# Optimization experiments

Measured on AMD Instinct MI355X. Metric: run time of the kernel, lower is better.

The kernel has to match this reference:

```python
import jax, jax.numpy as jnp
import numpy as np

B, IMG, P, D, H, HD, DEPTH, MLPD = 32, 224, 16, 768, 12, 64, 12, 3072
N = (IMG // P) ** 2 + 1  # 197 tokens incl. cls
TASKS, PL, NPL = 10, 5, 5
SCALE = HD ** -0.5


def _ln(x, w, b, eps=1e-6):
    m = jnp.mean(x, -1, keepdims=True)
    v = jnp.var(x, -1, keepdims=True)
    return (x - m) * jax.lax.rsqrt(v + eps) * w + b


def setup_inputs():
    key = jax.random.key(0)
    ks = jax.random.split(key, 16)
    g = lambda k, shape: (jax.random.normal(k, shape) * 0.02).astype(jnp.float32)
    return dict(
        x=jax.random.normal(ks[0], (B, 3, IMG, IMG), jnp.float32),
        task_id=jax.random.randint(ks[1], (B,), 0, TASKS),
        patch_w=g(ks[2], (D, 3, P, P)), patch_b=jnp.zeros((D,), jnp.float32),
        cls_token=g(ks[3], (1, 1, D)), pos_embed=g(ks[4], (1, N, D)),
        ln1_w=jnp.ones((DEPTH, D)), ln1_b=jnp.zeros((DEPTH, D)),
        qkv_w=g(ks[5], (DEPTH, 3 * D, D)), qkv_b=jnp.zeros((DEPTH, 3 * D)),
        proj_w=g(ks[6], (DEPTH, D, D)), proj_b=jnp.zeros((DEPTH, D)),
        ln2_w=jnp.ones((DEPTH, D)), ln2_b=jnp.zeros((DEPTH, D)),
        fc1_w=g(ks[7], (DEPTH, MLPD, D)), fc1_b=jnp.zeros((DEPTH, MLPD)),
        fc2_w=g(ks[8], (DEPTH, D, MLPD)), fc2_b=jnp.zeros((DEPTH, D)),
        norm_w=jnp.ones((D,)), norm_b=jnp.zeros((D,)),
        prefix_k=g(ks[9], (NPL, TASKS, PL, H, HD)),
        prefix_v=g(ks[10], (NPL, TASKS, PL, H, HD)),
        act_scale=jnp.ones((NPL, 2, 1, 1), jnp.float32),
    )


def reference(x, task_id, patch_w, patch_b, cls_token, pos_embed, ln1_w, ln1_b,
              qkv_w, qkv_b, proj_w, proj_b, ln2_w, ln2_b, fc1_w, fc1_b,
              fc2_w, fc2_b, norm_w, norm_b, prefix_k, prefix_v, act_scale):
    tid = jnp.clip(task_id, 0, TASKS - 1)
    Bx = x.shape[0]
    # patch embed: conv stride P -> [B, D, 14, 14] -> [B, 196, D]
    h = jax.lax.conv_general_dilated(x, patch_w, (P, P), 'VALID',
                                     dimension_numbers=('NCHW', 'OIHW', 'NCHW'))
    h = h.reshape(Bx, D, -1).transpose(0, 2, 1) + patch_b
    h = jnp.concatenate([jnp.broadcast_to(cls_token, (Bx, 1, D)), h], axis=1)
    h = h + pos_embed
    for i in range(DEPTH):
        xn = _ln(h, ln1_w[i], ln1_b[i])
        qkv = (xn @ qkv_w[i].T + qkv_b[i]).reshape(Bx, N, 3, H, HD)
        q, k, v = [jnp.transpose(qkv[:, :, j], (0, 2, 1, 3)) for j in range(3)]  # [B,H,N,HD]
        if i < NPL:
            kp = jnp.transpose(prefix_k[i][tid], (0, 2, 1, 3))  # [B,H,PL,HD]
            vp = jnp.transpose(prefix_v[i][tid], (0, 2, 1, 3))
            k = jnp.concatenate([kp, k], axis=2)
            v = jnp.concatenate([vp, v], axis=2)
        logits = jnp.einsum('bhqd,bhkd->bhqk', q, k) * SCALE
        if i < NPL:
            s = act_scale[i]  # [2,1,1]
            pp = logits[..., :PL]
            pp = pp + jax.nn.sigmoid(pp * s[0]) * s[1]  # norga gating on prefix logits
            logits = jnp.concatenate([pp, logits[..., PL:]], axis=-1)
        probs = jax.nn.softmax(logits, axis=-1)
        attn = jnp.einsum('bhqk,bhkd->bhqd', probs, v)
        attn = attn.transpose(0, 2, 1, 3).reshape(Bx, N, D)
        h = h + attn @ proj_w[i].T + proj_b[i]
        yn = _ln(h, ln2_w[i], ln2_b[i])
        y = jax.nn.gelu(yn @ fc1_w[i].T + fc1_b[i], approximate=False)
        h = h + y @ fc2_w[i].T + fc2_b[i]
    h = _ln(h, norm_w, norm_b)
    return h[:, 0]
```

## Files before the change

kernel.cpp:

```cpp
#include <hip/hip_runtime.h>
#include <hip/hip_bf16.h>

#define B_     32
#define NTOK   197
#define NPATCH 196
#define D_     768
#define H_     12
#define HD_    64
#define DEPTH_ 12
#define MLPD_  3072
#define TASKS_ 10
#define PL_    5
#define NPL_   5
#define SCALE_ 0.125f
#define ROWS   (B_*NTOK)
#define PSZ    (ROWS*D_)

typedef unsigned short ushortT;
typedef __bf16 bf16x8 __attribute__((ext_vector_type(8)));
typedef float  f32x4  __attribute__((ext_vector_type(4)));
typedef unsigned int u32x4 __attribute__((ext_vector_type(4)));

union FragU { u32x4 u; bf16x8 b; };

__device__ inline unsigned int f2bf(float f){
  unsigned int u = __float_as_uint(f);
  return (u + 0x7fffu + ((u >> 16) & 1u)) >> 16;
}
__device__ inline float bf2f(ushortT u){ return __uint_as_float(((unsigned)u) << 16); }
__device__ inline float gelu_f(float x){ return 0.5f * x * (1.f + erff(x * 0.70710678118f)); }

__device__ inline void gload16(const void* g, void* l){
  __builtin_amdgcn_global_load_lds(
      (const __attribute__((address_space(1))) void*)(uintptr_t)g,
      (__attribute__((address_space(3))) void*)(uintptr_t)l,
      16, 0, 0);
}

#define DSREAD(dst, addr, OFFS) \
  asm volatile("ds_read_b128 %0, %1 offset:" OFFS : "=v"(dst) : "v"(addr))

__global__ __launch_bounds__(256) void convw4_kernel(const float* __restrict__ s0,
    const float* __restrict__ s1, const float* __restrict__ s2, const float* __restrict__ s3,
    ushortT* __restrict__ dst)
{
  int idx = blockIdx.x * 256 + threadIdx.x;
  int e = idx * 8;
  if (e >= 7077888) return;
  const float* s; int loc;
  if (e < 1769472)      { s = s0; loc = e; }
  else if (e < 2359296) { s = s1; loc = e - 1769472; }
  else if (e < 4718592) { s = s2; loc = e - 2359296; }
  else                  { s = s3; loc = e - 4718592; }
  float4 a = *(const float4*)(s + loc);
  float4 c = *(const float4*)(s + loc + 4);
  uint4 o;
  o.x = f2bf(a.x) | (f2bf(a.y) << 16);
  o.y = f2bf(a.z) | (f2bf(a.w) << 16);
  o.z = f2bf(c.x) | (f2bf(c.y) << 16);
  o.w = f2bf(c.z) | (f2bf(c.w) << 16);
  *(uint4*)(dst + e) = o;
}

__global__ __launch_bounds__(256) void convw1_kernel(const float* __restrict__ s,
    ushortT* __restrict__ dst, int n8)
{
  int idx = blockIdx.x * 256 + threadIdx.x;
  if (idx >= n8) return;
  int e = idx * 8;
  float4 a = *(const float4*)(s + e);
  float4 c = *(const float4*)(s + e + 4);
  uint4 o;
  o.x = f2bf(a.x) | (f2bf(a.y) << 16);
  o.y = f2bf(a.z) | (f2bf(a.w) << 16);
  o.z = f2bf(c.x) | (f2bf(c.y) << 16);
  o.w = f2bf(c.z) | (f2bf(c.w) << 16);
  *(uint4*)(dst + e) = o;
}

__global__ __launch_bounds__(256) void im2col_kernel(const float* __restrict__ x,
                                                     ushortT* __restrict__ out)
{
  int idx = blockIdx.x * 256 + threadIdx.x;
  const int tot = B_ * NPATCH * D_;
  if (idx >= tot) return;
  int m = idx / D_, k = idx - m * D_;
  int b = m / NPATCH, p = m - b * NPATCH;
  int pr = p / 14, pc = p - pr * 14;
  int c = k >> 8, r = k & 255;
  int py = r >> 4, px = r & 15;
  float v = x[(((size_t)(b * 3 + c) * 224) + pr * 16 + py) * 224 + pc * 16 + px];
  out[idx] = (ushortT)f2bf(v);
}

__global__ __launch_bounds__(256) void assemble_ln_kernel(const float* __restrict__ pe,
    const float* __restrict__ patch_b, const float* __restrict__ cls,
    const float* __restrict__ pos, float* __restrict__ h,
    const float* __restrict__ lw, const float* __restrict__ lb,
    ushortT* __restrict__ y)
{
  const int row = blockIdx.x;
  const int b = row / NTOK, n = row - b * NTOK;
  const size_t base = (size_t)row * D_;
  const int t = threadIdx.x;
  float vals[3];
  float s = 0.f, ss = 0.f;
  #pragma unroll
  for (int e = 0; e < 3; e++) {
    int d = t + e * 256;
    float v;
    if (n == 0) v = cls[d];
    else        v = pe[((size_t)b * NPATCH + (n - 1)) * D_ + d] + patch_b[d];
    v += pos[(size_t)n * D_ + d];
    h[base + d] = v;
    vals[e] = v; s += v; ss += v * v;
  }
  #pragma unroll
  for (int off = 32; off >= 1; off >>= 1) {
    s  += __shfl_down(s, off);
    ss += __shfl_down(ss, off);
  }
  __shared__ float sm[4], ssm[4];
  int wid = t >> 6, lane = t & 63;
  if (lane == 0) { sm[wid] = s; ssm[wid] = ss; }
  __syncthreads();
  s  = sm[0] + sm[1] + sm[2] + sm[3];
  ss = ssm[0] + ssm[1] + ssm[2] + ssm[3];
  float mean = s * (1.f / D_);
  float var  = ss * (1.f / D_) - mean * mean;
  float inv  = rsqrtf(var + 1e-6f);
  #pragma unroll
  for (int e = 0; e < 3; e++) {
    int d = t + e * 256;
    y[base + d] = (ushortT)f2bf((vals[e] - mean) * inv * lw[d] + lb[d]);
  }
}

template<int NP, int DOLN>
__global__ __launch_bounds__(256) void reduce_ln_kernel(
    const ushortT* __restrict__ p, const float* __restrict__ bias,
    float* __restrict__ h, const float* __restrict__ lw,
    const float* __restrict__ lb, ushortT* __restrict__ y)
{
  const size_t base = (size_t)blockIdx.x * D_;
  const int t = threadIdx.x;
  float vals[3];
  float s = 0.f, ss = 0.f;
  #pragma unroll
  for (int e = 0; e < 3; e++) {
    int d = t + e * 256;
    size_t idx = base + d;
    float acc = h[idx] + bias[d];
    #pragma unroll
    for (int q = 0; q < NP; q++) acc += bf2f(p[(size_t)q * PSZ + idx]);
    h[idx] = acc;
    vals[e] = acc; s += acc; ss += acc * acc;
  }
  if (DOLN) {
    #pragma unroll
    for (int off = 32; off >= 1; off >>= 1) {
      s  += __shfl_down(s, off);
      ss += __shfl_down(ss, off);
    }
    __shared__ float sm[4], ssm[4];
    int wid = t >> 6, lane = t & 63;
    if (lane == 0) { sm[wid] = s; ssm[wid] = ss; }
    __syncthreads();
    s  = sm[0] + sm[1] + sm[2] + sm[3];
    ss = ssm[0] + ssm[1] + ssm[2] + ssm[3];
    float mean = s * (1.f / D_);
    float var  = ss * (1.f / D_) - mean * mean;
    float inv  = rsqrtf(var + 1e-6f);
    #pragma unroll
    for (int e = 0; e < 3; e++) {
      int d = t + e * 256;
      y[base + d] = (ushortT)f2bf((vals[e] - mean) * inv * lw[d] + lb[d]);
    }
  }
}

template<int OUTBF>
__global__ __launch_bounds__(256) void ln_kernel(const float* __restrict__ x, size_t xstride,
    const float* __restrict__ w, const float* __restrict__ b,
    void* __restrict__ y, size_t ystride)
{
  const float* xr = x + (size_t)blockIdx.x * xstride;
  float vals[3];
  float s = 0.f, ss = 0.f;
  #pragma unroll
  for (int t = 0; t < 3; t++) {
    float v = xr[threadIdx.x + t * 256];
    vals[t] = v; s += v; ss += v * v;
  }
  #pragma unroll
  for (int off = 32; off >= 1; off >>= 1) {
    s  += __shfl_down(s, off);
    ss += __shfl_down(ss, off);
  }
  __shared__ float sm[4], ssm[4];
  int wid = threadIdx.x >> 6, lane = threadIdx.x & 63;
  if (lane == 0) { sm[wid] = s; ssm[wid] = ss; }
  __syncthreads();
  s  = sm[0] + sm[1] + sm[2] + sm[3];
  ss = ssm[0] + ssm[1] + ssm[2] + ssm[3];
  float mean = s * (1.f / D_);
  float var  = ss * (1.f / D_) - mean * mean;
  float inv  = rsqrtf(var + 1e-6f);
  #pragma unroll
  for (int t = 0; t < 3; t++) {
    int d = threadIdx.x + t * 256;
    float v = (vals[t] - mean) * inv * w[d] + b[d];
    if (OUTBF) ((ushortT*)y)[(size_t)blockIdx.x * ystride + d] = (ushortT)f2bf(v);
    else       ((float*)y)  [(size_t)blockIdx.x * ystride + d] = v;
  }
}

template<int OUTBF, int ACT, int HASRES>
__global__ __launch_bounds__(256, 6) void gemm_mfma(
    const ushortT* __restrict__ A, const ushortT* __restrict__ W,
    const float* __restrict__ bias, const float* __restrict__ resid,
    void* __restrict__ Cout, int M, int N, int K, int LDA, int LDW)
{
  __shared__ ushortT lds[12288];
  const int tid = threadIdx.x, lane = tid & 63, wid = tid >> 6;
  const int bm = blockIdx.y * 128, bn = blockIdx.x * 64;
  const int wm = (wid >> 1) * 64, wn = (wid & 1) * 32;
  const int kz = blockIdx.z;
  A += (size_t)kz * K; W += (size_t)kz * K;
  char* Cb = (char*)Cout + (size_t)kz * M * N * (OUTBF ? 2 : 4);

  const int srow = lane >> 2;
  const int scol = ((lane & 3) ^ ((lane >> 3) & 3)) * 8;
  int arow0 = bm + (2 * wid) * 16 + srow;     if (arow0 > M - 1) arow0 = M - 1;
  int arow1 = bm + (2 * wid + 1) * 16 + srow; if (arow1 > M - 1) arow1 = M - 1;
  const int wrow = bn + wid * 16 + srow;
  const ushortT* aP0 = A + (size_t)arow0 * LDA + scol;
  const ushortT* aP1 = A + (size_t)arow1 * LDA + scol;
  const ushortT* wP0 = W + (size_t)wrow * LDW + scol;
  ushortT* sA = lds + 2 * wid * 512;
  ushortT* sW = lds + 8192 + wid * 512;

  f32x4 acc[4][2];
  #pragma unroll
  for (int i = 0; i < 4; i++)
    #pragma unroll
    for (int j = 0; j < 2; j++)
      acc[i][j] = (f32x4){0.f, 0.f, 0.f, 0.f};

  const int rsel = lane & 15, kc = lane >> 4;
  const unsigned ldsbase = (unsigned)(size_t)&lds[0];
  const unsigned rowoff = (unsigned)(rsel * 64 + ((kc ^ ((rsel >> 1) & 3)) << 4));
  const unsigned aBase = ldsbase + (unsigned)(wm * 64) + rowoff;
  const unsigned bBase = ldsbase + 16384u + (unsigned)(wn * 64) + rowoff;

  const int nk = K >> 5;

  #pragma unroll
  for (int p = 0; p < 2; ++p) {
    const int off = p * 32;
    gload16(aP0 + off, sA + p * 4096); gload16(aP1 + off, sA + p * 4096 + 512);
    gload16(wP0 + off, sW + p * 2048);
  }

  for (int kt = 0; kt < nk; ++kt) {
    const int cb = kt & 1;
    asm volatile("s_waitcnt vmcnt(3)" ::: "memory");
    __builtin_amdgcn_sched_barrier(0);
    __builtin_amdgcn_s_barrier();

    const unsigned aAddr = aBase + (unsigned)cb * 8192u;
    const unsigned bAddr = bBase + (unsigned)cb * 4096u;
    FragU fa0, fa1, fa2, fa3, fb0, fb1;
    DSREAD(fa0.u, aAddr, "0");
    DSREAD(fa1.u, aAddr, "1024");
    DSREAD(fa2.u, aAddr, "2048");
    DSREAD(fa3.u, aAddr, "3072");
    DSREAD(fb0.u, bAddr, "0");
    DSREAD(fb1.u, bAddr, "1024");
    asm volatile("s_waitcnt lgkmcnt(0)" ::: "memory");
    __builtin_amdgcn_sched_barrier(0);
    __builtin_amdgcn_s_barrier();

    const int nt = kt + 2;
    const int off = (nt < nk) ? nt * 32 : 0;
    gload16(aP0 + off, sA + cb * 4096); gload16(aP1 + off, sA + cb * 4096 + 512);
    gload16(wP0 + off, sW + cb * 2048);

    acc[0][0] = __builtin_amdgcn_mfma_f32_16x16x32_bf16(fa0.b, fb0.b, acc[0][0], 0, 0, 0);
    acc[0][1] = __builtin_amdgcn_mfma_f32_16x16x32_bf16(fa0.b, fb1.b, acc[0][1], 0, 0, 0);
    acc[1][0] = __builtin_amdgcn_mfma_f32_16x16x32_bf16(fa1.b, fb0.b, acc[1][0], 0, 0, 0);
    acc[1][1] = __builtin_amdgcn_mfma_f32_16x16x32_bf16(fa1.b, fb1.b, acc[1][1], 0, 0, 0);
    acc[2][0] = __builtin_amdgcn_mfma_f32_16x16x32_bf16(fa2.b, fb0.b, acc[2][0], 0, 0, 0);
    acc[2][1] = __builtin_amdgcn_mfma_f32_16x16x32_bf16(fa2.b, fb1.b, acc[2][1], 0, 0, 0);
    acc[3][0] = __builtin_amdgcn_mfma_f32_16x16x32_bf16(fa3.b, fb0.b, acc[3][0], 0, 0, 0);
    acc[3][1] = __builtin_amdgcn_mfma_f32_16x16x32_bf16(fa3.b, fb1.b, acc[3][1], 0, 0, 0);
  }

  const int crow = (lane >> 4) * 4, ccol = lane & 15;
  #pragma unroll
  for (int i = 0; i < 4; i++) {
    #pragma unroll
    for (int r = 0; r < 4; r++) {
      int m = bm + wm + i * 16 + crow + r;
      if (m < M) {
        #pragma unroll
        for (int j = 0; j < 2; j++) {
          int n = bn + wn + j * 16 + ccol;
          float v = acc[i][j][r];
          if (bias) v += bias[n];
          if (ACT) v = gelu_f(v);
          if (HASRES) v += resid[(size_t)m * N + n];
          if (OUTBF) ((ushortT*)Cb)[(size_t)m * N + n] = (ushortT)f2bf(v);
          else       ((float*)Cb)  [(size_t)m * N + n] = v;
        }
      }
    }
  }
  asm volatile("s_waitcnt vmcnt(0)" ::: "memory");
}

#define KROWS 208
#define VSTR  232
__global__ __launch_bounds__(256) void attn_mfma(
    const ushortT* __restrict__ qkv, const float* __restrict__ prefix_k,
    const float* __restrict__ prefix_v, const float* __restrict__ act_scale,
    const int* __restrict__ task_id, ushortT* __restrict__ out,
    int layer, int koff)
{
  __shared__ ushortT smem[13312 + 14848 + 4096];
  ushortT* Kl = smem;
  ushortT* Vt = smem + 13312;
  ushortT* Ps = smem + 13312 + 14848;

  const int tid = threadIdx.x, lane = tid & 63, wid = tid >> 6;
  const int g = lane >> 4, qc = lane & 15;
  const int qh = blockIdx.x, h = blockIdx.y, b = blockIdx.z;
  const int KtA = NTOK + koff;

  int tsk = 0;
  float s0 = 1.f, s1 = 1.f;
  if (koff) {
    tsk = task_id[b]; tsk = tsk < 0 ? 0 : (tsk > TASKS_ - 1 ? TASKS_ - 1 : tsk);
    s0 = act_scale[layer * 2]; s1 = act_scale[layer * 2 + 1];
  }

  {
    uint4* vz = (uint4*)Vt;
    for (int i = tid; i < 14848 / 8; i += 256) vz[i] = (uint4){0, 0, 0, 0};
    uint4* kz = (uint4*)(Kl + 202 * 64);
    if (tid < 48) kz[tid] = (uint4){0, 0, 0, 0};
  }
  __syncthreads();

  for (int u = tid; u < KtA * 8; u += 256) {
    int row = u >> 3, cg = u & 7;
    uint4 val;
    if (row < koff) {
      size_t off = ((((size_t)layer * TASKS_ + tsk) * PL_ + row) * H_ + h) * HD_ + cg * 8;
      float4 f0 = *(const float4*)(prefix_k + off);
      float4 f1 = *(const float4*)(prefix_k + off + 4);
      val.x = f2bf(f0.x) | (f2bf(f0.y) << 16); val.y = f2bf(f0.z) | (f2bf(f0.w) << 16);
      val.z = f2bf(f1.x) | (f2bf(f1.y) << 16); val.w = f2bf(f1.z) | (f2bf(f1.w) << 16);
    } else {
      int n = row - koff;
      val = *(const uint4*)(qkv + ((size_t)b * NTOK + n) * 2304 + D_ + h * HD_ + cg * 8);
    }
    *(uint4*)(Kl + row * 64 + ((cg * 8) ^ ((row & 7) << 3))) = val;
  }
  for (int u = tid; u < KtA * 8; u += 256) {
    int row = u >> 3, dg = u & 7;
    ushortT e[8];
    if (row < koff) {
      size_t off = ((((size_t)layer * TASKS_ + tsk) * PL_ + row) * H_ + h) * HD_ + dg * 8;
      #pragma unroll
      for (int t = 0; t < 8; t++) e[t] = (ushortT)f2bf(prefix_v[off + t]);
    } else {
      int n = row - koff;
      uint4 v = *(const uint4*)(qkv + ((size_t)b * NTOK + n) * 2304 + 2 * D_ + h * HD_ + dg * 8);
      *(uint4*)e = v;
    }
    #pragma unroll
    for (int t = 0; t < 8; t++) Vt[(dg * 8 + t) * VSTR + row] = e[t];
  }
  __syncthreads();

  const int tend = qh ? 13 : 7;
  for (int t = qh * 7 + wid; t < tend; t += 4) {
    const int q0 = t * 16;
    int qr = q0 + qc; if (qr > NTOK - 1) qr = NTOK - 1;
    const ushortT* qp = qkv + ((size_t)b * NTOK + qr) * 2304 + h * HD_ + g * 8;
    bf16x8 qf0 = *(const bf16x8*)qp;
    bf16x8 qf1 = *(const bf16x8*)(qp + 32);

    f32x4 sacc[13];
    #pragma unroll
    for (int kt = 0; kt < 13; kt++) sacc[kt] = (f32x4){0.f, 0.f, 0.f, 0.f};
    #pragma unroll
    for (int kt = 0; kt < 13; kt++) {
      int row = kt * 16 + qc;
      int sw = (row & 7) << 3;
      bf16x8 ka0 = *(const bf16x8*)(Kl + row * 64 + ((g * 8) ^ sw));
      bf16x8 ka1 = *(const bf16x8*)(Kl + row * 64 + ((32 + g * 8) ^ sw));
      sacc[kt] = __builtin_amdgcn_mfma_f32_16x16x32_bf16(ka0, qf0, sacc[kt], 0, 0, 0);
      sacc[kt] = __builtin_amdgcn_mfma_f32_16x16x32_bf16(ka1, qf1, sacc[kt], 0, 0, 0);
    }

    float* sp = (float*)sacc;
    float mx = -1e30f;
    #pragma unroll
    for (int kt = 0; kt < 13; kt++)
      #pragma unroll
      for (int r = 0; r < 4; r++) {
        int k = kt * 16 + g * 4 + r;
        float s = sp[kt * 4 + r] * SCALE_;
        if (koff && k < PL_) s += s1 / (1.f + __expf(-s * s0));
        if (k >= KtA) s = -1e30f;
        sp[kt * 4 + r] = s;
        mx = fmaxf(mx, s);
      }
    mx = fmaxf(mx, __shfl_xor(mx, 16));
    mx = fmaxf(mx, __shfl_xor(mx, 32));
    float sum = 0.f;
    #pragma unroll
    for (int i = 0; i < 52; i++) { float p = __expf(sp[i] - mx); sp[i] = p; sum += p; }
    sum += __shfl_xor(sum, 16);
    sum += __shfl_xor(sum, 32);
    const float inv = 1.f / sum;

    f32x4 oacc[4];
    #pragma unroll
    for (int d = 0; d < 4; d++) oacc[d] = (f32x4){0.f, 0.f, 0.f, 0.f};
    #pragma unroll
    for (int c = 0; c < 7; c++) {
      ushortT* slab = Ps + wid * 1024 + (c & 1) * 512;
      uint2 w0, w1;
      {
        float p0 = sp[8 * c + 0] * inv, p1 = sp[8 * c + 1] * inv;
        float p2 = sp[8 * c + 2] * inv, p3 = sp[8 * c + 3] * inv;
        w0.x = f2bf(p0) | (f2bf(p1) << 16); w0.y = f2bf(p2) | (f2bf(p3) << 16);
      }
      if (c < 6) {
        float p0 = sp[8 * c + 4] * inv, p1 = sp[8 * c + 5] * inv;
        float p2 = sp[8 * c + 6] * inv, p3 = sp[8 * c + 7] * inv;
        w1.x = f2bf(p0) | (f2bf(p1) << 16); w1.y = f2bf(p2) | (f2bf(p3) << 16);
      } else { w1.x = 0; w1.y = 0; }
      *(uint2*)(slab + qc * 32 + g * 4) = w0;
      *(uint2*)(slab + qc * 32 + 16 + g * 4) = w1;
      bf16x8 pa = *(const bf16x8*)(slab + qc * 32 + g * 8);
      #pragma unroll
      for (int dt = 0; dt < 4; dt++) {
        bf16x8 vb = *(const bf16x8*)(Vt + (dt * 16 + qc) * VSTR + c * 32 + g * 8);
        oacc[dt] = __builtin_amdgcn_mfma_f32_16x16x32_bf16(pa, vb, oacc[dt], 0, 0, 0);
      }
    }

    #pragma unroll
    for (int r = 0; r < 4; r++) {
      int q = q0 + g * 4 + r;
      if (q < NTOK) {
        size_t ro = ((size_t)b * NTOK + q) * D_ + h * HD_;
        #pragma unroll
        for (int dt = 0; dt < 4; dt++)
          out[ro + dt * 16 + qc] = (ushortT)f2bf(oacc[dt][r]);
      }
    }
  }
}

extern "C" void kernel_launch(void* const* d_in, const int* in_sizes, int n_in,
                              void* d_out, int out_size, void* d_ws, size_t ws_size,
                              hipStream_t stream)
{
  (void)in_sizes; (void)n_in; (void)out_size; (void)ws_size;
  const float* x         = (const float*)d_in[0];
  const int*   task_id   = (const int*)  d_in[1];
  const float* patch_w   = (const float*)d_in[2];
  const float* patch_b   = (const float*)d_in[3];
  const float* cls_token = (const float*)d_in[4];
  const float* pos_embed = (const float*)d_in[5];
  const float* ln1_w     = (const float*)d_in[6];
  const float* ln1_b     = (const float*)d_in[7];
  const float* qkv_w     = (const float*)d_in[8];
  const float* qkv_b     = (const float*)d_in[9];
  const float* proj_w    = (const float*)d_in[10];
  const float* proj_b    = (const float*)d_in[11];
  const float* ln2_w     = (const float*)d_in[12];
  const float* ln2_b     = (const float*)d_in[13];
  const float* fc1_w     = (const float*)d_in[14];
  const float* fc1_b     = (const float*)d_in[15];
  const float* fc2_w     = (const float*)d_in[16];
  const float* fc2_b     = (const float*)d_in[17];
  const float* norm_w    = (const float*)d_in[18];
  const float* norm_b    = (const float*)d_in[19];
  const float* prefix_k  = (const float*)d_in[20];
  const float* prefix_v  = (const float*)d_in[21];
  const float* act_scale = (const float*)d_in[22];
  float* out = (float*)d_out;

  char* wsb = (char*)d_ws;
  float*   h      = (float*)  (wsb);
  ushortT* actA   = (ushortT*)(wsb + 19365888);
  ushortT* qkvbuf = (ushortT*)(wsb + 29048832);
  ushortT* mlpbuf = (ushortT*)(wsb + 58097664);
  ushortT* wsc    = (ushortT*)(wsb + 96829440);
  float*   peout  = (float*)qkvbuf;

  ushortT* wqkv  = wsc;
  ushortT* wproj = wsc + 1769472;
  ushortT* wfc1  = wsc + 2359296;
  ushortT* wfc2  = wsc + 4718592;

  convw1_kernel<<<288, 256, 0, stream>>>(patch_w, wsc, 73728);
  im2col_kernel<<<(B_ * NPATCH * D_ + 255) / 256, 256, 0, stream>>>(x, actA);
  gemm_mfma<0,0,0><<<dim3(12, 49), 256, 0, stream>>>(
      actA, wsc, nullptr, nullptr, peout, B_ * NPATCH, D_, D_, D_, D_);
  assemble_ln_kernel<<<ROWS, 256, 0, stream>>>(
      peout, patch_b, cls_token, pos_embed, h, ln1_w, ln1_b, actA);

  for (int i = 0; i < DEPTH_; i++) {
    convw4_kernel<<<3456, 256, 0, stream>>>(
        qkv_w + (size_t)i * 1769472, proj_w + (size_t)i * 589824,
        fc1_w + (size_t)i * 2359296, fc2_w + (size_t)i * 2359296, wsc);
    gemm_mfma<1,0,0><<<dim3(36, 50), 256, 0, stream>>>(
        actA, wqkv, qkv_b + i * 3 * D_, nullptr, qkvbuf, ROWS, 3 * D_, D_, D_, D_);
    attn_mfma<<<dim3(2, H_, B_), 256, 0, stream>>>(
        qkvbuf, prefix_k, prefix_v, act_scale, task_id, actA, i, (i < NPL_) ? PL_ : 0);
    gemm_mfma<1,0,0><<<dim3(12, 50, 2), 256, 0, stream>>>(
        actA, wproj, nullptr, nullptr, qkvbuf, ROWS, D_, D_ / 2, D_, D_);
    reduce_ln_kernel<2,1><<<ROWS, 256, 0, stream>>>(
        qkvbuf, proj_b + i * D_, h, ln2_w + i * D_, ln2_b + i * D_, actA);
    gemm_mfma<1,1,0><<<dim3(48, 50), 256, 0, stream>>>(
        actA, wfc1, fc1_b + i * MLPD_, nullptr, mlpbuf, ROWS, MLPD_, D_, D_, D_);
    gemm_mfma<1,0,0><<<dim3(12, 50, 3), 256, 0, stream>>>(
        mlpbuf, wfc2, nullptr, nullptr, qkvbuf, ROWS, D_, MLPD_ / 3, MLPD_, MLPD_);
    if (i < DEPTH_ - 1) {
      reduce_ln_kernel<3,1><<<ROWS, 256, 0, stream>>>(
          qkvbuf, fc2_b + i * D_, h, ln1_w + (i + 1) * D_, ln1_b + (i + 1) * D_, actA);
    } else {
      reduce_ln_kernel<3,0><<<ROWS, 256, 0, stream>>>(
          qkvbuf, fc2_b + i * D_, h, nullptr, nullptr, nullptr);
    }
  }

  ln_kernel<0><<<B_, 256, 0, stream>>>(h, (size_t)NTOK * D_, norm_w, norm_b, out, D_);
}
```

Measured before the change: 3.175 ms.

## Load GEMM weight fragments directly from global into registers, bypassing LDS

The weight (B) operand of the MFMA GEMM now goes straight from global memory into register fragments, with a one-step register prefetch, instead of being staged through LDS. Only the A tile stays double-buffered in LDS, so shared memory per block drops and the two B ds_reads per k-step disappear. The cost is that each wave pair now loads the same weight columns redundantly from global/L2, with uncoalesced 16-byte per-lane loads whose latency sits closer to the MFMA issue. The vmcnt wait count is adjusted to fit the new mix of outstanding loads.

```diff
diff --git a/kernel.cpp b/kernel.cpp
--- a/kernel.cpp
+++ b/kernel.cpp
@@ -221,7 +221,7 @@
     const float* __restrict__ bias, const float* __restrict__ resid,
     void* __restrict__ Cout, int M, int N, int K, int LDA, int LDW)
 {
-  __shared__ ushortT lds[12288];
+  __shared__ ushortT lds[8192];
   const int tid = threadIdx.x, lane = tid & 63, wid = tid >> 6;
   const int bm = blockIdx.y * 128, bn = blockIdx.x * 64;
   const int wm = (wid >> 1) * 64, wn = (wid & 1) * 32;
@@ -233,12 +233,13 @@
   const int scol = ((lane & 3) ^ ((lane >> 3) & 3)) * 8;
   int arow0 = bm + (2 * wid) * 16 + srow;     if (arow0 > M - 1) arow0 = M - 1;
   int arow1 = bm + (2 * wid + 1) * 16 + srow; if (arow1 > M - 1) arow1 = M - 1;
-  const int wrow = bn + wid * 16 + srow;
   const ushortT* aP0 = A + (size_t)arow0 * LDA + scol;
   const ushortT* aP1 = A + (size_t)arow1 * LDA + scol;
-  const ushortT* wP0 = W + (size_t)wrow * LDW + scol;
   ushortT* sA = lds + 2 * wid * 512;
-  ushortT* sW = lds + 8192 + wid * 512;
+
+  const int rsel = lane & 15, kc = lane >> 4;
+  const ushortT* bp0 = W + (size_t)(bn + wn + rsel) * LDW + kc * 8;
+  const ushortT* bp1 = W + (size_t)(bn + wn + 16 + rsel) * LDW + kc * 8;
 
   f32x4 acc[4][2];
   #pragma unroll
@@ -247,53 +248,54 @@
     for (int j = 0; j < 2; j++)
       acc[i][j] = (f32x4){0.f, 0.f, 0.f, 0.f};
 
-  const int rsel = lane & 15, kc = lane >> 4;
   const unsigned ldsbase = (unsigned)(size_t)&lds[0];
-  const unsigned rowoff = (unsigned)(rsel * 64 + ((kc ^ ((rsel >> 1) & 3)) << 4));
-  const unsigned aBase = ldsbase + (unsigned)(wm * 64) + rowoff;
-  const unsigned bBase = ldsbase + 16384u + (unsigned)(wn * 64) + rowoff;
+  const unsigned aBase = ldsbase + (unsigned)(wm * 64) +
+      (unsigned)(rsel * 64 + ((kc ^ ((rsel >> 1) & 3)) << 4));
 
   const int nk = K >> 5;
 
-  #pragma unroll
-  for (int p = 0; p < 2; ++p) {
-    const int off = p * 32;
-    gload16(aP0 + off, sA + p * 4096); gload16(aP1 + off, sA + p * 4096 + 512);
-    gload16(wP0 + off, sW + p * 2048);
-  }
+  gload16(aP0, sA); gload16(aP1, sA + 512);
+  __builtin_amdgcn_sched_barrier(0);
+  FragU b0c, b1c, b0n, b1n;
+  b0c.u = *(const u32x4*)bp0;
+  b1c.u = *(const u32x4*)bp1;
+  __builtin_amdgcn_sched_barrier(0);
+  gload16(aP0 + 32, sA + 4096); gload16(aP1 + 32, sA + 4096 + 512);
 
   for (int kt = 0; kt < nk; ++kt) {
-    const int cb = kt & 1;
-    asm volatile("s_waitcnt vmcnt(3)" ::: "memory");
+    __builtin_amdgcn_sched_barrier(0);
+    asm volatile("s_waitcnt vmcnt(4)" ::: "memory");
     __builtin_amdgcn_sched_barrier(0);
     __builtin_amdgcn_s_barrier();
 
+    const int cb = kt & 1;
     const unsigned aAddr = aBase + (unsigned)cb * 8192u;
-    const unsigned bAddr = bBase + (unsigned)cb * 4096u;
-    FragU fa0, fa1, fa2, fa3, fb0, fb1;
+    FragU fa0, fa1, fa2, fa3;
     DSREAD(fa0.u, aAddr, "0");
     DSREAD(fa1.u, aAddr, "1024");
     DSREAD(fa2.u, aAddr, "2048");
     DSREAD(fa3.u, aAddr, "3072");
-    DSREAD(fb0.u, bAddr, "0");
-    DSREAD(fb1.u, bAddr, "1024");
     asm volatile("s_waitcnt lgkmcnt(0)" ::: "memory");
     __builtin_amdgcn_sched_barrier(0);
     __builtin_amdgcn_s_barrier();
 
+    const int ntB = (kt + 1 < nk) ? (kt + 1) * 32 : 0;
+    b0n.u = *(const u32x4*)(bp0 + ntB);
+    b1n.u = *(const u32x4*)(bp1 + ntB);
     const int nt = kt + 2;
     const int off = (nt < nk) ? nt * 32 : 0;
     gload16(aP0 + off, sA + cb * 4096); gload16(aP1 + off, sA + cb * 4096 + 512);
-    gload16(wP0 + off, sW + cb * 2048);
-
-    acc[0][0] = __builtin_amdgcn_mfma_f32_16x16x32_bf16(fa0.b, fb0.b, acc[0][0], 0, 0, 0);
-    acc[0][1] = __builtin_amdgcn_mfma_f32_16x16x32_bf16(fa0.b, fb1.b, acc[0][1], 0, 0, 0);
-    acc[1][0] = __builtin_amdgcn_mfma_f32_16x16x32_bf16(fa1.b, fb0.b, acc[1][0], 0, 0, 0);
-    acc[1][1] = __builtin_amdgcn_mfma_f32_16x16x32_bf16(fa1.b, fb1.b, acc[1][1], 0, 0, 0);
-    acc[2][0] = __builtin_amdgcn_mfma_f32_16x16x32_bf16(fa2.b, fb0.b, acc[2][0], 0, 0, 0);
-    acc[2][1] = __builtin_amdgcn_mfma_f32_16x16x32_bf16(fa2.b, fb1.b, acc[2][1], 0, 0, 0);
-    acc[3][0] = __builtin_amdgcn_mfma_f32_16x16x32_bf16(fa3.b, fb0.b, acc[3][0], 0, 0, 0);
-    acc[3][1] = __builtin_amdgcn_mfma_f32_16x16x32_bf16(fa3.b, fb1.b, acc[3][1], 0, 0, 0);
+
+    acc[0][0] = __builtin_amdgcn_mfma_f32_16x16x32_bf16(fa0.b, b0c.b, acc[0][0], 0, 0, 0);
+    acc[0][1] = __builtin_amdgcn_mfma_f32_16x16x32_bf16(fa0.b, b1c.b, acc[0][1], 0, 0, 0);
+    acc[1][0] = __builtin_amdgcn_mfma_f32_16x16x32_bf16(fa1.b, b0c.b, acc[1][0], 0, 0, 0);
+    acc[1][1] = __builtin_amdgcn_mfma_f32_16x16x32_bf16(fa1.b, b1c.b, acc[1][1], 0, 0, 0);
+    acc[2][0] = __builtin_amdgcn_mfma_f32_16x16x32_bf16(fa2.b, b0c.b, acc[2][0], 0, 0, 0);
+    acc[2][1] = __builtin_amdgcn_mfma_f32_16x16x32_bf16(fa2.b, b1c.b, acc[2][1], 0, 0, 0);
+    acc[3][0] = __builtin_amdgcn_mfma_f32_16x16x32_bf16(fa3.b, b0c.b, acc[3][0], 0, 0, 0);
+    acc[3][1] = __builtin_amdgcn_mfma_f32_16x16x32_bf16(fa3.b, b1c.b, acc[3][1], 0, 0, 0);
+
+    b0c = b0n; b1c = b1n;
   }
 
   const int crow = (lane >> 4) * 4, ccol = lane & 15;
```

Result: slower. 4.177 ms (+31.5%).
